# Optimization experiments

Measured on AMD Instinct MI355X. Metric: run time of the kernel, lower is better.

The kernel has to match this reference:

```python
import jax, jax.numpy as jnp
import numpy as np

N_NODES = 100000
N_EDGES = 1600000
D = 64
K1 = 10   # conv1 hops
K2 = 3    # stacked conv hops


def _gcn_norm(edge_index, num_nodes, dtype):
    # PyG gcn_norm with add_self_loops=False: sym normalization D^-1/2 A D^-1/2
    row, col = edge_index[0], edge_index[1]
    deg = jax.ops.segment_sum(jnp.ones(row.shape, dtype), col, num_segments=num_nodes)
    dinv = jnp.where(deg > 0, jax.lax.rsqrt(jnp.maximum(deg, 1.0)), 0.0)
    return dinv[row] * dinv[col]  # [E]


def _tagconv(x, ws, b, row, col, nrm, num_nodes):
    # out = sum_k (A_hat^k x) @ W_k + b ; ws: [K+1, D, D]
    out = x @ ws[0]
    h = x
    for k in range(1, ws.shape[0]):
        msg = h[row] * nrm[:, None]                       # [E, D] gather
        h = jax.ops.segment_sum(msg, col, num_segments=num_nodes)  # [N, D] scatter-add
        out = out + h @ ws[k]
    return out + b


def setup_inputs() -> dict:
    key = jax.random.key(0)
    ks = jax.random.split(key, 8)
    x = jax.random.normal(ks[0], (N_NODES, D), dtype=jnp.float32)
    edge_index = jax.random.randint(ks[1], (2, N_EDGES), 0, N_NODES, dtype=jnp.int64)
    s = 1.0 / np.sqrt(D)
    w1 = jax.random.normal(ks[2], (K1 + 1, D, D), dtype=jnp.float32) * s
    b1 = jnp.zeros((D,), dtype=jnp.float32)
    w2 = jax.random.normal(ks[3], (K2 + 1, D, D), dtype=jnp.float32) * s
    b2 = jnp.zeros((D,), dtype=jnp.float32)
    wc = jax.random.normal(ks[4], (D, D), dtype=jnp.float32) * s
    bc = jnp.zeros((D,), dtype=jnp.float32)
    return {"x": x, "edge_index": edge_index, "w1": w1, "b1": b1,
            "w2": w2, "b2": b2, "wc": wc, "bc": bc}


def reference(x, edge_index, w1, b1, w2, b2, wc, bc):
    num_nodes = x.shape[0]
    row, col = edge_index[0], edge_index[1]
    nrm = _gcn_norm(edge_index, num_nodes, x.dtype)
    h = jnp.tanh(_tagconv(x, w1, b1, row, col, nrm, num_nodes))
    h = jnp.tanh(_tagconv(h, w2, b2, row, col, nrm, num_nodes))
    return h @ wc + bc
```

## Files before the change

### kernel.cpp

```cpp
#include <hip/hip_runtime.h>
#include <hip/hip_bf16.h>

#define PAD 16
#define NBKT_MAX 512

typedef __attribute__((ext_vector_type(8))) short short8;
typedef __attribute__((ext_vector_type(4))) float float4v;

__device__ __forceinline__ short8 as_s8(uint4 v) {
    union { uint4 u; short8 s; } x; x.u = v; return x.s;
}

__device__ __forceinline__ int pad_up(int v) { return (v + (PAD - 1)) & ~(PAD - 1); }


__global__ __launch_bounds__(256) void hist_kernel(const int* __restrict__ col,
                                                   int* __restrict__ blockHist, int E, int nbkt) {
    __shared__ int h[NBKT_MAX];
    for (int i = threadIdx.x; i < nbkt; i += 256) h[i] = 0;
    __syncthreads();
    int chunk = (E + gridDim.x - 1) / gridDim.x;
    int lo = blockIdx.x * chunk, hi = min(lo + chunk, E);
    for (int e = lo + threadIdx.x; e < hi; e += 256) atomicAdd(&h[col[e] >> 9], 1);
    __syncthreads();
    for (int i = threadIdx.x; i < nbkt; i += 256) blockHist[i * 256 + blockIdx.x] = h[i];
}

__global__ __launch_bounds__(256) void bscan_kernel(int* __restrict__ blockHist,
                                                    int* __restrict__ bktTot, int nbkt) {
    __shared__ int a[256], b[256];
    int bkt = blockIdx.x;
    int t = threadIdx.x;
    int v = blockHist[bkt * 256 + t];
    a[t] = v;
    __syncthreads();
    int* s = a; int* d = b;
    for (int off = 1; off < 256; off <<= 1) {
        int x = s[t];
        if (t >= off) x += s[t - off];
        d[t] = x;
        __syncthreads();
        int* tmp = s; s = d; d = tmp;
    }
    blockHist[bkt * 256 + t] = s[t] - v;
    if (t == 255) bktTot[bkt] = s[t];
}

__global__ void scan_small(const int* __restrict__ in, int* __restrict__ outp, int n) {
    __shared__ int a[256], b[256];
    int t = threadIdx.x;
    int v = t < n ? in[t] : 0;
    a[t] = v;
    __syncthreads();
    int* s = a; int* d = b;
    for (int off = 1; off < 256; off <<= 1) {
        int x = s[t];
        if (t >= off) x += s[t - off];
        d[t] = x;
        __syncthreads();
        int* tmp = s; s = d; d = tmp;
    }
    if (t < n) outp[t] = s[t] - v;
}

__global__ __launch_bounds__(256) void scatter_kernel(const int* __restrict__ row,
                                                      const int* __restrict__ col,
                                                      const int* __restrict__ blockHist,
                                                      const int* __restrict__ bktOff,
                                                      int2* __restrict__ pairs, int E, int nbkt) {
    __shared__ int cur[NBKT_MAX];
    for (int i = threadIdx.x; i < nbkt; i += 256)
        cur[i] = bktOff[i] + blockHist[i * 256 + blockIdx.x];
    __syncthreads();
    int chunk = (E + gridDim.x - 1) / gridDim.x;
    int lo = blockIdx.x * chunk, hi = min(lo + chunk, E);
    for (int e = lo + threadIdx.x; e < hi; e += 256) {
        int dn = col[e];
        int p = atomicAdd(&cur[dn >> 9], 1);
        pairs[p] = make_int2(row[e], dn);
    }
}

__global__ __launch_bounds__(256) void deg_pairs_kernel(
        const int2* __restrict__ pairs, const int* __restrict__ bktOff,
        const int* __restrict__ bktTot,
        int* __restrict__ deg, float* __restrict__ dinv, float* __restrict__ dinv2,
        float* __restrict__ sdeg, int N) {
    __shared__ int cnt[512];
    int b = blockIdx.x, d0 = b << 9;
    for (int i = threadIdx.x; i < 512; i += 256) cnt[i] = 0;
    __syncthreads();
    int lo = bktOff[b], hi = lo + bktTot[b];
    for (int p = lo + threadIdx.x; p < hi; p += 256)
        atomicAdd(&cnt[pairs[p].y - d0], 1);
    __syncthreads();
    for (int i = threadIdx.x; i < 512; i += 256) {
        int d = d0 + i;
        if (d < N) {
            int c = cnt[i];
            deg[d] = c;
            float v = c > 0 ? rsqrtf((float)c) : 0.0f;
            dinv[d] = v;
            dinv2[d] = v * v;
            sdeg[d] = c > 0 ? sqrtf((float)c) : 0.0f;
        }
    }
}

__global__ void scan_phaseA(const int* __restrict__ deg, int* __restrict__ chunkSum, int N) {
    int t = threadIdx.x;
    int idx = blockIdx.x * 512 + t;
    int v = idx < N ? pad_up(deg[idx]) : 0;
    for (int o = 32; o > 0; o >>= 1) v += __shfl_down(v, o, 64);
    __shared__ int wsum[8];
    if ((t & 63) == 0) wsum[t >> 6] = v;
    __syncthreads();
    if (t == 0) {
        int s = 0;
        for (int i = 0; i < 8; ++i) s += wsum[i];
        chunkSum[blockIdx.x] = s;
    }
}

__global__ void scan_phaseC(const int* __restrict__ deg, const int* __restrict__ chunkOff,
                            int* __restrict__ rowptr, int N) {
    __shared__ int a[512], b[512];
    int t = threadIdx.x;
    int idx = blockIdx.x * 512 + t;
    int v = idx < N ? pad_up(deg[idx]) : 0;
    a[t] = v;
    __syncthreads();
    int* s = a; int* d = b;
    for (int off = 1; off < 512; off <<= 1) {
        int x = s[t];
        if (t >= off) x += s[t - off];
        d[t] = x;
        __syncthreads();
        int* tmp = s; s = d; d = tmp;
    }
    if (idx < N) rowptr[idx] = chunkOff[blockIdx.x] + s[t] - v;
    if (idx == N - 1) rowptr[N] = chunkOff[blockIdx.x] + s[t];
}

__global__ __launch_bounds__(256) void cluster_kernel(const int2* __restrict__ pairs,
                                                      const int* __restrict__ bktOff,
                                                      const int* __restrict__ bktTot,
                                                      const int* __restrict__ rowptr,
                                                      int* __restrict__ srcs, int N) {
    __shared__ int cur[512];
    int b = blockIdx.x;
    int d0 = b << 9;
    for (int i = threadIdx.x; i < 512; i += 256) {
        int d = d0 + i;
        cur[i] = (d < N) ? rowptr[d] : 0;
    }
    __syncthreads();
    int lo = bktOff[b], hi = lo + bktTot[b];
    for (int p = lo + threadIdx.x; p < hi; p += 256) {
        int2 e = pairs[p];
        int pos = atomicAdd(&cur[e.y - d0], 1);
        srcs[pos] = e.x;
    }
    __syncthreads();
    for (int i = threadIdx.x; i < 512; i += 256) {
        int d = d0 + i;
        if (d < N) {
            int p = cur[i];
            int p1 = rowptr[d + 1];
            for (; p < p1; ++p) srcs[p] = N;
        }
    }
}


__global__ void wcvt_kernel(const float* __restrict__ w1, const float* __restrict__ w2,
                            const float* __restrict__ wc, __hip_bfloat16* __restrict__ wf) {
    int idx = blockIdx.x * blockDim.x + threadIdx.x;
    if (idx >= 16 * 4096) return;
    int g = idx >> 12, r = idx & 4095;
    int j = r & 7, lane = (r >> 3) & 63, u = (r >> 9) & 3, t = r >> 11;
    int k = t * 32 + (lane >> 4) * 8 + j;
    int n = u * 16 + (lane & 15);
    const float* W = (g < 11) ? (w1 + (size_t)g * 4096)
                  : (g < 15) ? (w2 + (size_t)(g - 11) * 4096) : wc;
    wf[idx] = __float2bfloat16(W[k * 64 + n]);
}

__global__ void zero_pads_kernel(__hip_bfloat16* __restrict__ gbase, size_t gstride,
                                 int nbuf, int N) {
    int i = blockIdx.x * blockDim.x + threadIdx.x;
    int b = i >> 6;
    if (b < nbuf) gbase[(size_t)b * gstride + (size_t)N * 64 + (i & 63)] = __float2bfloat16(0.0f);
}

__global__ void cvt_g_kernel(const float* __restrict__ x, const float* __restrict__ dinv,
                             __hip_bfloat16* __restrict__ g, int N) {
    int i = blockIdx.x * blockDim.x + threadIdx.x;
    if (i < N * 64) g[i] = __float2bfloat16(dinv[i >> 6] * x[i]);
}


__global__ __launch_bounds__(256) void hop_kernel(
        const __hip_bfloat16* __restrict__ g_in,
        const int* __restrict__ srcs, const int* __restrict__ rowptr,
        const float* __restrict__ dinv2,
        __hip_bfloat16* __restrict__ g_out, int n) {
    const int lane = threadIdx.x & 63;
    const int quad = lane >> 4;
    const int c4 = lane & 15;
    int gw = __builtin_amdgcn_readfirstlane((blockIdx.x * blockDim.x + threadIdx.x) >> 6);
    int nw = (gridDim.x * blockDim.x) >> 6;
    for (int d = gw; d < n; d += nw) {
        int p0 = rowptr[d], p1 = rowptr[d + 1];
        float a0 = 0.f, a1 = 0.f, a2 = 0.f, a3 = 0.f;
        for (int p = p0; p < p1; p += 16) {
            int4 sq = ((const int4*)(srcs + p))[quad];
            const uint2* r0 = (const uint2*)(g_in + (size_t)sq.x * 64);
            const uint2* r1 = (const uint2*)(g_in + (size_t)sq.y * 64);
            const uint2* r2 = (const uint2*)(g_in + (size_t)sq.z * 64);
            const uint2* r3 = (const uint2*)(g_in + (size_t)sq.w * 64);
            uint2 v0 = r0[c4], v1 = r1[c4], v2 = r2[c4], v3 = r3[c4];
            a0 += __uint_as_float(v0.x << 16); a1 += __uint_as_float(v0.x & 0xffff0000u);
            a2 += __uint_as_float(v0.y << 16); a3 += __uint_as_float(v0.y & 0xffff0000u);
            a0 += __uint_as_float(v1.x << 16); a1 += __uint_as_float(v1.x & 0xffff0000u);
            a2 += __uint_as_float(v1.y << 16); a3 += __uint_as_float(v1.y & 0xffff0000u);
            a0 += __uint_as_float(v2.x << 16); a1 += __uint_as_float(v2.x & 0xffff0000u);
            a2 += __uint_as_float(v2.y << 16); a3 += __uint_as_float(v2.y & 0xffff0000u);
            a0 += __uint_as_float(v3.x << 16); a1 += __uint_as_float(v3.x & 0xffff0000u);
            a2 += __uint_as_float(v3.y << 16); a3 += __uint_as_float(v3.y & 0xffff0000u);
        }
        a0 += __shfl_xor(a0, 16); a1 += __shfl_xor(a1, 16);
        a2 += __shfl_xor(a2, 16); a3 += __shfl_xor(a3, 16);
        a0 += __shfl_xor(a0, 32); a1 += __shfl_xor(a1, 32);
        a2 += __shfl_xor(a2, 32); a3 += __shfl_xor(a3, 32);
        if (quad == 0) {
            float s = dinv2[d];
            union { __hip_bfloat16 h[4]; uint2 u; } pk;
            pk.h[0] = __float2bfloat16(s * a0);
            pk.h[1] = __float2bfloat16(s * a1);
            pk.h[2] = __float2bfloat16(s * a2);
            pk.h[3] = __float2bfloat16(s * a3);
            ((uint2*)(g_out + (size_t)d * 64))[c4] = pk.u;
        }
    }
}


template<int NG>
__global__ __launch_bounds__(256) void final_kernel(
        const __hip_bfloat16* gbase, size_t gstride,
        const __hip_bfloat16* __restrict__ wf,
        const float* __restrict__ sdeg, const float* __restrict__ bias,
        const float* __restrict__ scale,
        __hip_bfloat16* out16, int ntiles) {
    const int lane = threadIdx.x & 63;
    const int col = lane & 15, quad = lane >> 4;
    int wv = (blockIdx.x * blockDim.x + threadIdx.x) >> 6;
    int nwv = (gridDim.x * blockDim.x) >> 6;
    const uint4* wfq = (const uint4*)wf;
    for (int tile = wv; tile < ntiles; tile += nwv) {
        int base = tile * 16;
        float4v acc0 = {0.f, 0.f, 0.f, 0.f};
        float4v acc1 = {0.f, 0.f, 0.f, 0.f};
        float4v acc2 = {0.f, 0.f, 0.f, 0.f};
        float4v acc3 = {0.f, 0.f, 0.f, 0.f};
#pragma unroll
        for (int g = 0; g < NG; ++g) {
            const uint4* ga = (const uint4*)(gbase + (size_t)g * gstride);
            const uint4* wg = wfq + (size_t)g * 512;
#pragma unroll
            for (int t = 0; t < 2; ++t) {
                short8 a = as_s8(ga[(size_t)(base + col) * 8 + t * 4 + quad]);
                short8 b0 = as_s8(wg[(t * 4 + 0) * 64 + lane]);
                short8 b1 = as_s8(wg[(t * 4 + 1) * 64 + lane]);
                short8 b2 = as_s8(wg[(t * 4 + 2) * 64 + lane]);
                short8 b3 = as_s8(wg[(t * 4 + 3) * 64 + lane]);
                acc0 = __builtin_amdgcn_mfma_f32_16x16x32_bf16(a, b0, acc0, 0, 0, 0);
                acc1 = __builtin_amdgcn_mfma_f32_16x16x32_bf16(a, b1, acc1, 0, 0, 0);
                acc2 = __builtin_amdgcn_mfma_f32_16x16x32_bf16(a, b2, acc2, 0, 0, 0);
                acc3 = __builtin_amdgcn_mfma_f32_16x16x32_bf16(a, b3, acc3, 0, 0, 0);
            }
        }
#pragma unroll
        for (int r = 0; r < 4; ++r) {
            int nd = base + quad * 4 + r;
            float sd = sdeg[nd];
            float sc = scale ? scale[nd] : 1.0f;
            float f0 = sc * tanhf(sd * acc0[r] + bias[0 * 16 + col]);
            float f1 = sc * tanhf(sd * acc1[r] + bias[1 * 16 + col]);
            float f2 = sc * tanhf(sd * acc2[r] + bias[2 * 16 + col]);
            float f3 = sc * tanhf(sd * acc3[r] + bias[3 * 16 + col]);
            out16[(size_t)nd * 64 + 0 * 16 + col] = __float2bfloat16(f0);
            out16[(size_t)nd * 64 + 1 * 16 + col] = __float2bfloat16(f1);
            out16[(size_t)nd * 64 + 2 * 16 + col] = __float2bfloat16(f2);
            out16[(size_t)nd * 64 + 3 * 16 + col] = __float2bfloat16(f3);
        }
    }
}


__global__ __launch_bounds__(256) void head_kernel(
        const __hip_bfloat16* __restrict__ v16, const __hip_bfloat16* __restrict__ wfc,
        const float* __restrict__ bc, float* __restrict__ out, int ntiles) {
    const int lane = threadIdx.x & 63;
    const int col = lane & 15, quad = lane >> 4;
    int wv = (blockIdx.x * blockDim.x + threadIdx.x) >> 6;
    int nwv = (gridDim.x * blockDim.x) >> 6;
    const uint4* va = (const uint4*)v16;
    const uint4* wg = (const uint4*)wfc;
    for (int tile = wv; tile < ntiles; tile += nwv) {
        int base = tile * 16;
        float4v acc0 = {0.f, 0.f, 0.f, 0.f};
        float4v acc1 = {0.f, 0.f, 0.f, 0.f};
        float4v acc2 = {0.f, 0.f, 0.f, 0.f};
        float4v acc3 = {0.f, 0.f, 0.f, 0.f};
#pragma unroll
        for (int t = 0; t < 2; ++t) {
            short8 a = as_s8(va[(size_t)(base + col) * 8 + t * 4 + quad]);
            short8 b0 = as_s8(wg[(t * 4 + 0) * 64 + lane]);
            short8 b1 = as_s8(wg[(t * 4 + 1) * 64 + lane]);
            short8 b2 = as_s8(wg[(t * 4 + 2) * 64 + lane]);
            short8 b3 = as_s8(wg[(t * 4 + 3) * 64 + lane]);
            acc0 = __builtin_amdgcn_mfma_f32_16x16x32_bf16(a, b0, acc0, 0, 0, 0);
            acc1 = __builtin_amdgcn_mfma_f32_16x16x32_bf16(a, b1, acc1, 0, 0, 0);
            acc2 = __builtin_amdgcn_mfma_f32_16x16x32_bf16(a, b2, acc2, 0, 0, 0);
            acc3 = __builtin_amdgcn_mfma_f32_16x16x32_bf16(a, b3, acc3, 0, 0, 0);
        }
#pragma unroll
        for (int r = 0; r < 4; ++r) {
            int nd = base + quad * 4 + r;
            out[(size_t)nd * 64 + 0 * 16 + col] = acc0[r] + bc[0 * 16 + col];
            out[(size_t)nd * 64 + 1 * 16 + col] = acc1[r] + bc[1 * 16 + col];
            out[(size_t)nd * 64 + 2 * 16 + col] = acc2[r] + bc[2 * 16 + col];
            out[(size_t)nd * 64 + 3 * 16 + col] = acc3[r] + bc[3 * 16 + col];
        }
    }
}


extern "C" void kernel_launch(void* const* d_in, const int* in_sizes, int n_in,
                              void* d_out, int out_size, void* d_ws, size_t ws_size,
                              hipStream_t stream) {
    const float* x  = (const float*)d_in[0];
    const int*   ei = (const int*)d_in[1];
    const float* w1 = (const float*)d_in[2];
    const float* b1 = (const float*)d_in[3];
    const float* w2 = (const float*)d_in[4];
    const float* b2 = (const float*)d_in[5];
    const float* wc = (const float*)d_in[6];
    const float* bc = (const float*)d_in[7];
    float* out = (float*)d_out;

    const int N = in_sizes[0] / 64;
    const int E = in_sizes[1] / 2;
    const int K1 = 10, K2 = 3;
    const int* row = ei;
    const int* col = ei + E;
    const int Epad = E + (PAD - 1) * N + 64;
    const int NBUF = 11;
    const int nbkt = (N + 511) >> 9;
    const size_t gstride = (((size_t)(N + 1) * 64) + 127) & ~(size_t)127;

    char* base = (char*)d_ws;
    auto alloc = [&](size_t bytes) { void* p = (void*)base; base += (bytes + 255) & ~(size_t)255; return p; };
    int*   deg      = (int*)alloc((size_t)N * 4);
    int*   rowptr   = (int*)alloc((size_t)(N + 1) * 4);
    int*   chunkSum = (int*)alloc(256 * 4);
    int*   chunkOff = (int*)alloc(256 * 4);
    int*   blockHist= (int*)alloc((size_t)NBKT_MAX * 256 * 4);
    int*   bktTot   = (int*)alloc((size_t)NBKT_MAX * 4);
    int*   bktOff   = (int*)alloc((size_t)NBKT_MAX * 4);
    float* dinv     = (float*)alloc((size_t)N * 4);
    float* dinv2    = (float*)alloc((size_t)N * 4);
    float* sdeg     = (float*)alloc((size_t)N * 4);
    int*   srcs     = (int*)alloc((size_t)Epad * 4);
    __hip_bfloat16* wf    = (__hip_bfloat16*)alloc((size_t)16 * 4096 * 2);
    __hip_bfloat16* gbase = (__hip_bfloat16*)alloc((size_t)NBUF * gstride * 2);

    auto G = [&](int k) { return gbase + (size_t)k * gstride; };
    int2* pairs = (int2*)G(9);
    __hip_bfloat16* vbuf16 = G(5);

    const int numChunks = (N + 511) / 512;
    const int xBlocks = (N * 64 + 255) / 256;
    const int gBlocks = 2048;
    const int ntiles = (N + 15) / 16;

    hist_kernel<<<256, 256, 0, stream>>>(col, blockHist, E, nbkt);
    bscan_kernel<<<nbkt, 256, 0, stream>>>(blockHist, bktTot, nbkt);
    scan_small<<<1, 256, 0, stream>>>(bktTot, bktOff, nbkt);
    scatter_kernel<<<256, 256, 0, stream>>>(row, col, blockHist, bktOff, pairs, E, nbkt);
    deg_pairs_kernel<<<nbkt, 256, 0, stream>>>(pairs, bktOff, bktTot, deg, dinv, dinv2, sdeg, N);
    scan_phaseA<<<numChunks, 512, 0, stream>>>(deg, chunkSum, N);
    scan_small<<<1, 256, 0, stream>>>(chunkSum, chunkOff, numChunks);
    scan_phaseC<<<numChunks, 512, 0, stream>>>(deg, chunkOff, rowptr, N);
    cluster_kernel<<<nbkt, 256, 0, stream>>>(pairs, bktOff, bktTot, rowptr, srcs, N);

    wcvt_kernel<<<(16 * 4096 + 255) / 256, 256, 0, stream>>>(w1, w2, wc, wf);
    zero_pads_kernel<<<(NBUF * 64 + 255) / 256, 256, 0, stream>>>(gbase, gstride, NBUF, N);
    cvt_g_kernel<<<xBlocks, 256, 0, stream>>>(x, dinv, G(0), N);

    for (int k = 1; k <= K1; ++k)
        hop_kernel<<<gBlocks, 256, 0, stream>>>(G(k - 1), srcs, rowptr, dinv2, G(k), N);

    final_kernel<11><<<gBlocks, 256, 0, stream>>>(gbase, gstride, wf, sdeg, b1, dinv,
                                                  G(1), ntiles);

    for (int k = 1; k <= K2; ++k)
        hop_kernel<<<gBlocks, 256, 0, stream>>>(G(k), srcs, rowptr, dinv2, G(k + 1), N);

    final_kernel<4><<<gBlocks, 256, 0, stream>>>(G(1), gstride, wf + (size_t)11 * 4096,
                                                 sdeg, b2, nullptr, vbuf16, ntiles);

    head_kernel<<<gBlocks, 256, 0, stream>>>(vbuf16, wf + (size_t)15 * 4096, bc, out, ntiles);
}
```

Measured before the change: 669.3 us.

## Process two destination nodes per wave in hop and two tiles per wave in final

The hop kernel now has each wave handle two destination rows at once, interleaving their gathers to raise memory-level parallelism. Exhausted rows are padded with index n, which relies on the zero pad row. The final kernel computes two 16-row tiles per wave so the weight fragments are reused, and it adds launch bounds with occupancy 4 and an unroll-1 group loop. The final and head grids are resized to one tile or pair per wave. The cost is more register pressure and wasted lanes when the two rows' degrees differ.

```diff
diff --git a/kernel.cpp b/kernel.cpp
--- a/kernel.cpp
+++ b/kernel.cpp
@@ -210,44 +210,77 @@
     const int c4 = lane & 15;
     int gw = __builtin_amdgcn_readfirstlane((blockIdx.x * blockDim.x + threadIdx.x) >> 6);
     int nw = (gridDim.x * blockDim.x) >> 6;
-    for (int d = gw; d < n; d += nw) {
-        int p0 = rowptr[d], p1 = rowptr[d + 1];
+    for (int d = gw * 2; d < n; d += nw * 2) {
+        int dA = d;
+        int dB = d + 1;
+        bool hasB = dB < n;
+        int pA = rowptr[dA], eA = rowptr[dA + 1];
+        int pB = hasB ? rowptr[dB] : 0;
+        int eB = hasB ? rowptr[dB + 1] : 0;
         float a0 = 0.f, a1 = 0.f, a2 = 0.f, a3 = 0.f;
-        for (int p = p0; p < p1; p += 16) {
-            int4 sq = ((const int4*)(srcs + p))[quad];
-            const uint2* r0 = (const uint2*)(g_in + (size_t)sq.x * 64);
-            const uint2* r1 = (const uint2*)(g_in + (size_t)sq.y * 64);
-            const uint2* r2 = (const uint2*)(g_in + (size_t)sq.z * 64);
-            const uint2* r3 = (const uint2*)(g_in + (size_t)sq.w * 64);
-            uint2 v0 = r0[c4], v1 = r1[c4], v2 = r2[c4], v3 = r3[c4];
-            a0 += __uint_as_float(v0.x << 16); a1 += __uint_as_float(v0.x & 0xffff0000u);
-            a2 += __uint_as_float(v0.y << 16); a3 += __uint_as_float(v0.y & 0xffff0000u);
-            a0 += __uint_as_float(v1.x << 16); a1 += __uint_as_float(v1.x & 0xffff0000u);
-            a2 += __uint_as_float(v1.y << 16); a3 += __uint_as_float(v1.y & 0xffff0000u);
-            a0 += __uint_as_float(v2.x << 16); a1 += __uint_as_float(v2.x & 0xffff0000u);
-            a2 += __uint_as_float(v2.y << 16); a3 += __uint_as_float(v2.y & 0xffff0000u);
-            a0 += __uint_as_float(v3.x << 16); a1 += __uint_as_float(v3.x & 0xffff0000u);
-            a2 += __uint_as_float(v3.y << 16); a3 += __uint_as_float(v3.y & 0xffff0000u);
+        float b0 = 0.f, b1 = 0.f, b2 = 0.f, b3 = 0.f;
+        while (pA < eA || pB < eB) {
+            int4 sqA, sqB;
+            if (pA < eA) { sqA = ((const int4*)(srcs + pA))[quad]; pA += 16; }
+            else sqA = make_int4(n, n, n, n);
+            if (pB < eB) { sqB = ((const int4*)(srcs + pB))[quad]; pB += 16; }
+            else sqB = make_int4(n, n, n, n);
+            uint2 vA0 = ((const uint2*)(g_in + (size_t)sqA.x * 64))[c4];
+            uint2 vA1 = ((const uint2*)(g_in + (size_t)sqA.y * 64))[c4];
+            uint2 vA2 = ((const uint2*)(g_in + (size_t)sqA.z * 64))[c4];
+            uint2 vA3 = ((const uint2*)(g_in + (size_t)sqA.w * 64))[c4];
+            uint2 vB0 = ((const uint2*)(g_in + (size_t)sqB.x * 64))[c4];
+            uint2 vB1 = ((const uint2*)(g_in + (size_t)sqB.y * 64))[c4];
+            uint2 vB2 = ((const uint2*)(g_in + (size_t)sqB.z * 64))[c4];
+            uint2 vB3 = ((const uint2*)(g_in + (size_t)sqB.w * 64))[c4];
+            a0 += __uint_as_float(vA0.x << 16); a1 += __uint_as_float(vA0.x & 0xffff0000u);
+            a2 += __uint_as_float(vA0.y << 16); a3 += __uint_as_float(vA0.y & 0xffff0000u);
+            a0 += __uint_as_float(vA1.x << 16); a1 += __uint_as_float(vA1.x & 0xffff0000u);
+            a2 += __uint_as_float(vA1.y << 16); a3 += __uint_as_float(vA1.y & 0xffff0000u);
+            a0 += __uint_as_float(vA2.x << 16); a1 += __uint_as_float(vA2.x & 0xffff0000u);
+            a2 += __uint_as_float(vA2.y << 16); a3 += __uint_as_float(vA2.y & 0xffff0000u);
+            a0 += __uint_as_float(vA3.x << 16); a1 += __uint_as_float(vA3.x & 0xffff0000u);
+            a2 += __uint_as_float(vA3.y << 16); a3 += __uint_as_float(vA3.y & 0xffff0000u);
+            b0 += __uint_as_float(vB0.x << 16); b1 += __uint_as_float(vB0.x & 0xffff0000u);
+            b2 += __uint_as_float(vB0.y << 16); b3 += __uint_as_float(vB0.y & 0xffff0000u);
+            b0 += __uint_as_float(vB1.x << 16); b1 += __uint_as_float(vB1.x & 0xffff0000u);
+            b2 += __uint_as_float(vB1.y << 16); b3 += __uint_as_float(vB1.y & 0xffff0000u);
+            b0 += __uint_as_float(vB2.x << 16); b1 += __uint_as_float(vB2.x & 0xffff0000u);
+            b2 += __uint_as_float(vB2.y << 16); b3 += __uint_as_float(vB2.y & 0xffff0000u);
+            b0 += __uint_as_float(vB3.x << 16); b1 += __uint_as_float(vB3.x & 0xffff0000u);
+            b2 += __uint_as_float(vB3.y << 16); b3 += __uint_as_float(vB3.y & 0xffff0000u);
         }
         a0 += __shfl_xor(a0, 16); a1 += __shfl_xor(a1, 16);
         a2 += __shfl_xor(a2, 16); a3 += __shfl_xor(a3, 16);
         a0 += __shfl_xor(a0, 32); a1 += __shfl_xor(a1, 32);
         a2 += __shfl_xor(a2, 32); a3 += __shfl_xor(a3, 32);
+        b0 += __shfl_xor(b0, 16); b1 += __shfl_xor(b1, 16);
+        b2 += __shfl_xor(b2, 16); b3 += __shfl_xor(b3, 16);
+        b0 += __shfl_xor(b0, 32); b1 += __shfl_xor(b1, 32);
+        b2 += __shfl_xor(b2, 32); b3 += __shfl_xor(b3, 32);
         if (quad == 0) {
-            float s = dinv2[d];
+            float s = dinv2[dA];
             union { __hip_bfloat16 h[4]; uint2 u; } pk;
             pk.h[0] = __float2bfloat16(s * a0);
             pk.h[1] = __float2bfloat16(s * a1);
             pk.h[2] = __float2bfloat16(s * a2);
             pk.h[3] = __float2bfloat16(s * a3);
-            ((uint2*)(g_out + (size_t)d * 64))[c4] = pk.u;
+            ((uint2*)(g_out + (size_t)dA * 64))[c4] = pk.u;
+        } else if (quad == 1 && hasB) {
+            float s = dinv2[dB];
+            union { __hip_bfloat16 h[4]; uint2 u; } pk;
+            pk.h[0] = __float2bfloat16(s * b0);
+            pk.h[1] = __float2bfloat16(s * b1);
+            pk.h[2] = __float2bfloat16(s * b2);
+            pk.h[3] = __float2bfloat16(s * b3);
+            ((uint2*)(g_out + (size_t)dB * 64))[c4] = pk.u;
         }
     }
 }
 
 
 template<int NG>
-__global__ __launch_bounds__(256) void final_kernel(
+__global__ __launch_bounds__(256, 4) void final_kernel(
         const __hip_bfloat16* gbase, size_t gstride,
         const __hip_bfloat16* __restrict__ wf,
         const float* __restrict__ sdeg, const float* __restrict__ bias,
@@ -258,42 +291,68 @@
     int wv = (blockIdx.x * blockDim.x + threadIdx.x) >> 6;
     int nwv = (gridDim.x * blockDim.x) >> 6;
     const uint4* wfq = (const uint4*)wf;
-    for (int tile = wv; tile < ntiles; tile += nwv) {
-        int base = tile * 16;
-        float4v acc0 = {0.f, 0.f, 0.f, 0.f};
-        float4v acc1 = {0.f, 0.f, 0.f, 0.f};
-        float4v acc2 = {0.f, 0.f, 0.f, 0.f};
-        float4v acc3 = {0.f, 0.f, 0.f, 0.f};
-#pragma unroll
+    int npairs = (ntiles + 1) >> 1;
+    for (int pr = wv; pr < npairs; pr += nwv) {
+        int tile1 = pr * 2;
+        int tile2 = tile1 + 1;
+        bool has2 = tile2 < ntiles;
+        int ba = tile1 * 16;
+        int bb = (has2 ? tile2 : tile1) * 16;
+        float4v accA0 = {0.f, 0.f, 0.f, 0.f}, accA1 = {0.f, 0.f, 0.f, 0.f};
+        float4v accA2 = {0.f, 0.f, 0.f, 0.f}, accA3 = {0.f, 0.f, 0.f, 0.f};
+        float4v accB0 = {0.f, 0.f, 0.f, 0.f}, accB1 = {0.f, 0.f, 0.f, 0.f};
+        float4v accB2 = {0.f, 0.f, 0.f, 0.f}, accB3 = {0.f, 0.f, 0.f, 0.f};
+#pragma unroll 1
         for (int g = 0; g < NG; ++g) {
             const uint4* ga = (const uint4*)(gbase + (size_t)g * gstride);
             const uint4* wg = wfq + (size_t)g * 512;
 #pragma unroll
             for (int t = 0; t < 2; ++t) {
-                short8 a = as_s8(ga[(size_t)(base + col) * 8 + t * 4 + quad]);
-                short8 b0 = as_s8(wg[(t * 4 + 0) * 64 + lane]);
-                short8 b1 = as_s8(wg[(t * 4 + 1) * 64 + lane]);
-                short8 b2 = as_s8(wg[(t * 4 + 2) * 64 + lane]);
-                short8 b3 = as_s8(wg[(t * 4 + 3) * 64 + lane]);
-                acc0 = __builtin_amdgcn_mfma_f32_16x16x32_bf16(a, b0, acc0, 0, 0, 0);
-                acc1 = __builtin_amdgcn_mfma_f32_16x16x32_bf16(a, b1, acc1, 0, 0, 0);
-                acc2 = __builtin_amdgcn_mfma_f32_16x16x32_bf16(a, b2, acc2, 0, 0, 0);
-                acc3 = __builtin_amdgcn_mfma_f32_16x16x32_bf16(a, b3, acc3, 0, 0, 0);
+                short8 aA = as_s8(ga[(size_t)(ba + col) * 8 + t * 4 + quad]);
+                short8 aB = as_s8(ga[(size_t)(bb + col) * 8 + t * 4 + quad]);
+                short8 w0 = as_s8(wg[(t * 4 + 0) * 64 + lane]);
+                short8 w1 = as_s8(wg[(t * 4 + 1) * 64 + lane]);
+                short8 w2 = as_s8(wg[(t * 4 + 2) * 64 + lane]);
+                short8 w3 = as_s8(wg[(t * 4 + 3) * 64 + lane]);
+                accA0 = __builtin_amdgcn_mfma_f32_16x16x32_bf16(aA, w0, accA0, 0, 0, 0);
+                accB0 = __builtin_amdgcn_mfma_f32_16x16x32_bf16(aB, w0, accB0, 0, 0, 0);
+                accA1 = __builtin_amdgcn_mfma_f32_16x16x32_bf16(aA, w1, accA1, 0, 0, 0);
+                accB1 = __builtin_amdgcn_mfma_f32_16x16x32_bf16(aB, w1, accB1, 0, 0, 0);
+                accA2 = __builtin_amdgcn_mfma_f32_16x16x32_bf16(aA, w2, accA2, 0, 0, 0);
+                accB2 = __builtin_amdgcn_mfma_f32_16x16x32_bf16(aB, w2, accB2, 0, 0, 0);
+                accA3 = __builtin_amdgcn_mfma_f32_16x16x32_bf16(aA, w3, accA3, 0, 0, 0);
+                accB3 = __builtin_amdgcn_mfma_f32_16x16x32_bf16(aB, w3, accB3, 0, 0, 0);
             }
         }
 #pragma unroll
         for (int r = 0; r < 4; ++r) {
-            int nd = base + quad * 4 + r;
+            int nd = ba + quad * 4 + r;
             float sd = sdeg[nd];
             float sc = scale ? scale[nd] : 1.0f;
-            float f0 = sc * tanhf(sd * acc0[r] + bias[0 * 16 + col]);
-            float f1 = sc * tanhf(sd * acc1[r] + bias[1 * 16 + col]);
-            float f2 = sc * tanhf(sd * acc2[r] + bias[2 * 16 + col]);
-            float f3 = sc * tanhf(sd * acc3[r] + bias[3 * 16 + col]);
+            float f0 = sc * tanhf(sd * accA0[r] + bias[0 * 16 + col]);
+            float f1 = sc * tanhf(sd * accA1[r] + bias[1 * 16 + col]);
+            float f2 = sc * tanhf(sd * accA2[r] + bias[2 * 16 + col]);
+            float f3 = sc * tanhf(sd * accA3[r] + bias[3 * 16 + col]);
             out16[(size_t)nd * 64 + 0 * 16 + col] = __float2bfloat16(f0);
             out16[(size_t)nd * 64 + 1 * 16 + col] = __float2bfloat16(f1);
             out16[(size_t)nd * 64 + 2 * 16 + col] = __float2bfloat16(f2);
             out16[(size_t)nd * 64 + 3 * 16 + col] = __float2bfloat16(f3);
+        }
+        if (has2) {
+#pragma unroll
+            for (int r = 0; r < 4; ++r) {
+                int nd = bb + quad * 4 + r;
+                float sd = sdeg[nd];
+                float sc = scale ? scale[nd] : 1.0f;
+                float f0 = sc * tanhf(sd * accB0[r] + bias[0 * 16 + col]);
+                float f1 = sc * tanhf(sd * accB1[r] + bias[1 * 16 + col]);
+                float f2 = sc * tanhf(sd * accB2[r] + bias[2 * 16 + col]);
+                float f3 = sc * tanhf(sd * accB3[r] + bias[3 * 16 + col]);
+                out16[(size_t)nd * 64 + 0 * 16 + col] = __float2bfloat16(f0);
+                out16[(size_t)nd * 64 + 1 * 16 + col] = __float2bfloat16(f1);
+                out16[(size_t)nd * 64 + 2 * 16 + col] = __float2bfloat16(f2);
+                out16[(size_t)nd * 64 + 3 * 16 + col] = __float2bfloat16(f3);
+            }
         }
     }
 }
@@ -385,6 +444,9 @@
     const int xBlocks = (N * 64 + 255) / 256;
     const int gBlocks = 2048;
     const int ntiles = (N + 15) / 16;
+    const int npairs = (ntiles + 1) / 2;
+    const int fBlocks = (npairs + 3) / 4;
+    const int hBlocks = (ntiles + 3) / 4;
 
     hist_kernel<<<256, 256, 0, stream>>>(col, blockHist, E, nbkt);
     bscan_kernel<<<nbkt, 256, 0, stream>>>(blockHist, bktTot, nbkt);
@@ -403,14 +465,14 @@
     for (int k = 1; k <= K1; ++k)
         hop_kernel<<<gBlocks, 256, 0, stream>>>(G(k - 1), srcs, rowptr, dinv2, G(k), N);
 
-    final_kernel<11><<<gBlocks, 256, 0, stream>>>(gbase, gstride, wf, sdeg, b1, dinv,
+    final_kernel<11><<<fBlocks, 256, 0, stream>>>(gbase, gstride, wf, sdeg, b1, dinv,
                                                   G(1), ntiles);
 
     for (int k = 1; k <= K2; ++k)
         hop_kernel<<<gBlocks, 256, 0, stream>>>(G(k), srcs, rowptr, dinv2, G(k + 1), N);
 
-    final_kernel<4><<<gBlocks, 256, 0, stream>>>(G(1), gstride, wf + (size_t)11 * 4096,
+    final_kernel<4><<<fBlocks, 256, 0, stream>>>(G(1), gstride, wf + (size_t)11 * 4096,
                                                  sdeg, b2, nullptr, vbuf16, ntiles);
 
-    head_kernel<<<gBlocks, 256, 0, stream>>>(vbuf16, wf + (size_t)15 * 4096, bc, out, ntiles);
-}
+    head_kernel<<<hBlocks, 256, 0, stream>>>(vbuf16, wf + (size_t)15 * 4096, bc, out, ntiles);
+}
```

After: 666.0 us. Within noise of the previous version (-0.5%).
